# Optimization experiments

Hardware: AMD Instinct MI355X
Metric: run time of the kernel (lower is better)

Reference implementation:

```python
import jax, jax.numpy as jnp
import numpy as np
from math import sqrt

B, L, D, NH = 1, 2048, 1024, 16
HD = D // NH
EPS = 1e-5
NEG = -1e9


def setup_inputs() -> dict:
    key = jax.random.key(0)
    ks = jax.random.split(key, 5)
    x = jax.random.normal(ks[0], (B, L, D), jnp.float32)
    # causal additive mask (added to raw QK^T scores before /sqrt(d))
    causal = jnp.tril(jnp.ones((L, L), bool))
    m = jnp.where(causal, 0.0, NEG).astype(jnp.float32)[None, None]  # (1,1,L,L)
    init = lambda k, s: (0.02 * jax.random.normal(k, s)).astype(jnp.float32)
    return dict(
        x=x, m=m,
        wx_w=init(ks[1], (3 * D, D)), wx_b=jnp.zeros((3 * D,), jnp.float32),
        wo_w=init(ks[2], (D, D)), wo_b=jnp.zeros((D,), jnp.float32),
        ffn1_w=init(ks[3], (4 * D, D)), ffn1_b=jnp.zeros((4 * D,), jnp.float32),
        ffn2_w=init(ks[4], (D, 4 * D)), ffn2_b=jnp.zeros((D,), jnp.float32),
        ln1_w=jnp.float32(1.0), ln1_b=jnp.float32(0.0),
        ln2_w=jnp.float32(1.0), ln2_b=jnp.float32(0.0),
    )


def layer_norm(x, w, b):
    # scalar gain/bias, biased variance via E[x^2] - E[x]^2 (as in source)
    mu = x.mean(-1, keepdims=True)
    mu2 = (x * x).mean(-1, keepdims=True)
    sigma = jnp.sqrt(mu2 - mu * mu + EPS)
    return w * (x - mu) / sigma + b


def gelu(x):
    return x * 0.5 * (1 + jax.scipy.special.erf(x / sqrt(2.0)))


def reference(x, m, wx_w, wx_b, wo_w, wo_b, ffn1_w, ffn1_b, ffn2_w, ffn2_b,
              ln1_w, ln1_b, ln2_w, ln2_b):
    b, l, d = x.shape
    qkv = layer_norm(x, ln1_w, ln1_b) @ wx_w.T + wx_b          # (b,l,3d)
    q, k, v = [t.reshape(b, l, NH, HD) for t in jnp.split(qkv, 3, axis=-1)]
    # mask added BEFORE scaling by 1/sqrt(d) -- faithful to source
    scores = (jnp.einsum('bind,bjnd->bnij', q, k) + m) / sqrt(d)  # (b,nh,l,l)
    A = jax.nn.softmax(scores, axis=-1)
    mha = jnp.einsum('bnij,bjnd->bind', A, v).reshape(b, l, d)
    x = x + mha @ wo_w.T + wo_b
    h = layer_norm(x, ln2_w, ln2_b)
    return x + gelu(h @ ffn1_w.T + ffn1_b) @ ffn2_w.T + ffn2_b
```

## Files before the change

### kernel.cpp

```cpp
#include <hip/hip_runtime.h>

typedef short bf16x8 __attribute__((ext_vector_type(8)));
typedef float f32x4 __attribute__((ext_vector_type(4)));
typedef unsigned short u16;

__device__ __forceinline__ u16 f2b(float f) {
  unsigned u = __builtin_bit_cast(unsigned, f);
  u += 0x7fffu + ((u >> 16) & 1u);
  return (u16)(u >> 16);
}
__device__ __forceinline__ float b2f(u16 h) {
  unsigned u = ((unsigned)h) << 16;
  return __builtin_bit_cast(float, u);
}

__device__ __forceinline__ void gload16(const void* g, void* l) {
  __builtin_amdgcn_global_load_lds(
      (const __attribute__((address_space(1))) unsigned*)g,
      (__attribute__((address_space(3))) unsigned*)l, 16, 0, 0);
}

__global__ __launch_bounds__(256) void prep_kernel(
    const float* __restrict__ s0, int n0, const float* __restrict__ s1, int n1,
    const float* __restrict__ s2, int n2, const float* __restrict__ s3, int n3,
    u16* __restrict__ d0, u16* __restrict__ d1, u16* __restrict__ d2, u16* __restrict__ d3,
    const float* __restrict__ x, u16* __restrict__ lnout,
    const float* __restrict__ wp, const float* __restrict__ bp) {
  __shared__ float red[8];
  if (blockIdx.x < 1024) {
    long long total = ((long long)n0 + n1 + n2 + n3) >> 2;
    long long stride = 1024LL * 256;
    for (long long i = (long long)blockIdx.x * 256 + threadIdx.x; i < total; i += stride) {
      long long e = i << 2;
      const float* sp; u16* dp; long long off;
      if (e < n0)                { sp = s0; dp = d0; off = e; }
      else if (e < n0 + n1)      { sp = s1; dp = d1; off = e - n0; }
      else if (e < n0 + n1 + n2) { sp = s2; dp = d2; off = e - n0 - n1; }
      else                       { sp = s3; dp = d3; off = e - n0 - n1 - n2; }
      float4 v = *(const float4*)(sp + off);
      ushort4 o;
      o.x = f2b(v.x); o.y = f2b(v.y); o.z = f2b(v.z); o.w = f2b(v.w);
      *(ushort4*)(dp + off) = o;
    }
    return;
  }
  int row = blockIdx.x - 1024;
  const float* xr = x + (size_t)row * 1024;
  float4 v = ((const float4*)xr)[threadIdx.x];
  float lsum = v.x + v.y + v.z + v.w;
  float lsq = v.x * v.x + v.y * v.y + v.z * v.z + v.w * v.w;
#pragma unroll
  for (int off = 32; off; off >>= 1) {
    lsum += __shfl_down(lsum, off);
    lsq += __shfl_down(lsq, off);
  }
  int wv_ = threadIdx.x >> 6, ln_ = threadIdx.x & 63;
  if (ln_ == 0) { red[wv_] = lsum; red[4 + wv_] = lsq; }
  __syncthreads();
  if (threadIdx.x == 0) {
    float ts = red[0] + red[1] + red[2] + red[3];
    float ts2 = red[4] + red[5] + red[6] + red[7];
    red[0] = ts; red[4] = ts2;
  }
  __syncthreads();
  float mu = red[0] * (1.0f / 1024.0f);
  float mu2 = red[4] * (1.0f / 1024.0f);
  float inv = 1.0f / sqrtf(mu2 - mu * mu + 1e-5f);
  float gw = *wp, gb = *bp;
  ushort4 o;
  o.x = f2b(gw * (v.x - mu) * inv + gb);
  o.y = f2b(gw * (v.y - mu) * inv + gb);
  o.z = f2b(gw * (v.z - mu) * inv + gb);
  o.w = f2b(gw * (v.w - mu) * inv + gb);
  ((ushort4*)lnout)[(size_t)row * 256 + threadIdx.x] = o;
}

__global__ __launch_bounds__(256) void reduce2(
    const float* __restrict__ p, const float* __restrict__ bias,
    const float* __restrict__ resid, float* __restrict__ out) {
  int i = blockIdx.x * 256 + threadIdx.x;
  float4 a = ((const float4*)p)[i];
  float4 b = ((const float4*)p)[i + 524288];
  float4 r = ((const float4*)resid)[i];
  float4 bb = ((const float4*)bias)[i & 255];
  float4 o;
  o.x = a.x + b.x + r.x + bb.x;
  o.y = a.y + b.y + r.y + bb.y;
  o.z = a.z + b.z + r.z + bb.z;
  o.w = a.w + b.w + r.w + bb.w;
  ((float4*)out)[i] = o;
}

__global__ __launch_bounds__(256) void reduce_ln(
    const float* __restrict__ p, const float* __restrict__ bias,
    const float* __restrict__ resid, float* __restrict__ x1out,
    u16* __restrict__ lnout,
    const float* __restrict__ wp, const float* __restrict__ bp) {
  int row = blockIdx.x;
  int i = row * 256 + threadIdx.x;
  float4 a = ((const float4*)p)[i];
  float4 b = ((const float4*)p)[i + 524288];
  float4 r = ((const float4*)resid)[i];
  float4 bb = ((const float4*)bias)[threadIdx.x];
  float4 v;
  v.x = a.x + b.x + r.x + bb.x;
  v.y = a.y + b.y + r.y + bb.y;
  v.z = a.z + b.z + r.z + bb.z;
  v.w = a.w + b.w + r.w + bb.w;
  ((float4*)x1out)[i] = v;
  float lsum = v.x + v.y + v.z + v.w;
  float lsq = v.x * v.x + v.y * v.y + v.z * v.z + v.w * v.w;
#pragma unroll
  for (int off = 32; off; off >>= 1) {
    lsum += __shfl_down(lsum, off);
    lsq += __shfl_down(lsq, off);
  }
  __shared__ float red[8];
  int wv_ = threadIdx.x >> 6, ln_ = threadIdx.x & 63;
  if (ln_ == 0) { red[wv_] = lsum; red[4 + wv_] = lsq; }
  __syncthreads();
  if (threadIdx.x == 0) {
    float ts = red[0] + red[1] + red[2] + red[3];
    float ts2 = red[4] + red[5] + red[6] + red[7];
    red[0] = ts; red[4] = ts2;
  }
  __syncthreads();
  float mu = red[0] * (1.0f / 1024.0f);
  float mu2 = red[4] * (1.0f / 1024.0f);
  float inv = 1.0f / sqrtf(mu2 - mu * mu + 1e-5f);
  float gw = *wp, gb = *bp;
  ushort4 o;
  o.x = f2b(gw * (v.x - mu) * inv + gb);
  o.y = f2b(gw * (v.y - mu) * inv + gb);
  o.z = f2b(gw * (v.z - mu) * inv + gb);
  o.w = f2b(gw * (v.w - mu) * inv + gb);
  ((ushort4*)lnout)[i] = o;
}

#define BN 128
#define BK 64

template <int EPI, int BMT, bool SPLITX>
__global__ __launch_bounds__(256, (BMT == 128 ? 2 : 3)) void gemm_bt(
    const u16* __restrict__ A, const u16* __restrict__ W,
    const float* __restrict__ bias, const float* __restrict__ resid,
    void* __restrict__ Cout, u16* __restrict__ vtout, int M, int N, int K) {
  constexpr int MR = BMT / 32;
  __shared__ __align__(16) u16 sA[2][BMT * BK];
  __shared__ __align__(16) u16 sB[2][BN * BK];
  const int tid = threadIdx.x;

  const int gx = gridDim.x, gy = gridDim.y;
  int bx, by;
  {
    int oxy = blockIdx.y * gx + blockIdx.x;
    int xcd = oxy & 7, pos = oxy >> 3;
    if (SPLITX) {
      int bxp = gx >> 3;
      bx = xcd * bxp + pos % bxp;
      by = pos / bxp;
    } else {
      int byp = gy >> 3;
      by = xcd * byp + pos % byp;
      bx = pos / byp;
    }
  }

  const int l = tid & 63;
  const int w = tid >> 6;
  const int wm = w >> 1, wn = w & 1;
  const int lr = l & 15, lg = l >> 4;

  f32x4 acc[MR][4] = {};

  const int r_st = tid >> 3;
  const int s_st = tid & 7;

  const u16* Abase = A + (size_t)(by * BMT) * K;
  const u16* Wbase = W + (size_t)(bx * BN) * K;
  const int NK = K / (BK * (int)gridDim.z);
  const int ktbase = (int)blockIdx.z * NK;

  auto stage = [&](int buf, int kt) {
    const int k0 = (ktbase + kt) * BK;
#pragma unroll
    for (int i = 0; i < BMT / 32; i++) {
      int r = i * 32 + r_st;
      int ss = s_st ^ (r & 7);
      gload16(Abase + (size_t)r * K + k0 + ss * 8, &sA[buf][(i * 256 + tid) * 8]);
    }
#pragma unroll
    for (int i = 0; i < 4; i++) {
      int r = i * 32 + r_st;
      int ss = s_st ^ (r & 7);
      gload16(Wbase + (size_t)r * K + k0 + ss * 8, &sB[buf][(i * 256 + tid) * 8]);
    }
  };

  auto compute = [&](int buf) {
#pragma unroll
    for (int kk = 0; kk < 2; kk++) {
      bf16x8 a[MR], b[4];
#pragma unroll
      for (int mr = 0; mr < MR; mr++) {
        int row = wm * (BMT / 2) + mr * 16 + lr;
        int ss = (kk * 4 + lg) ^ (row & 7);
        a[mr] = *(const bf16x8*)&sA[buf][row * 64 + ss * 8];
      }
#pragma unroll
      for (int nr = 0; nr < 4; nr++) {
        int row = wn * 64 + nr * 16 + lr;
        int ss = (kk * 4 + lg) ^ (row & 7);
        b[nr] = *(const bf16x8*)&sB[buf][row * 64 + ss * 8];
      }
#pragma unroll
      for (int mr = 0; mr < MR; mr++)
#pragma unroll
        for (int nr = 0; nr < 4; nr++)
          acc[mr][nr] = __builtin_amdgcn_mfma_f32_16x16x32_bf16(a[mr], b[nr], acc[mr][nr], 0, 0, 0);
    }
  };

  stage(0, 0);
  asm volatile("s_waitcnt vmcnt(0)" ::: "memory");
  __syncthreads();
  for (int kt = 0; kt < NK; kt++) {
    if (kt + 1 < NK) stage((kt + 1) & 1, kt + 1);
    compute(kt & 1);
    asm volatile("s_waitcnt vmcnt(0)" ::: "memory");
    __syncthreads();
  }

  const int crow0 = by * BMT + wm * (BMT / 2);
  const int ccol0 = bx * BN + wn * 64;

  if (EPI == 4) {
    float* P4 = (float*)Cout + (size_t)blockIdx.z * (size_t)M * N;
#pragma unroll
    for (int nr = 0; nr < 4; nr++) {
      int col = ccol0 + nr * 16 + lr;
#pragma unroll
      for (int mr = 0; mr < MR; mr++) {
        int rowb = crow0 + mr * 16 + lg * 4;
#pragma unroll
        for (int r = 0; r < 4; r++)
          P4[(size_t)(rowb + r) * N + col] = acc[mr][nr][r];
      }
    }
    return;
  }

  if (EPI == 3 && ccol0 >= 2048) {
    const int hd0 = ccol0 - 2048;
#pragma unroll
    for (int nr = 0; nr < 4; nr++) {
      int hd = hd0 + nr * 16 + lr;
      float bv = bias[ccol0 + nr * 16 + lr];
#pragma unroll
      for (int mr = 0; mr < MR; mr++) {
        int m0 = crow0 + mr * 16 + lg * 4;
        ushort4 o;
        o.x = f2b(acc[mr][nr][0] + bv);
        o.y = f2b(acc[mr][nr][1] + bv);
        o.z = f2b(acc[mr][nr][2] + bv);
        o.w = f2b(acc[mr][nr][3] + bv);
        *(ushort4*)&vtout[(size_t)hd * 2048 + m0] = o;
      }
    }
    return;
  }

#pragma unroll
  for (int nr = 0; nr < 4; nr++) {
    int col = ccol0 + nr * 16 + lr;
    float bv = bias[col];
#pragma unroll
    for (int mr = 0; mr < MR; mr++) {
      int rowb = crow0 + mr * 16 + lg * 4;
#pragma unroll
      for (int r = 0; r < 4; r++) {
        float v = acc[mr][nr][r] + bv;
        size_t off = (size_t)(rowb + r) * N + col;
        if (EPI == 2) {
          float u = 0.7978845608f * (v + 0.044715f * v * v * v);
          u = fminf(15.0f, fmaxf(-15.0f, u));
          float e = __expf(2.0f * u);
          float g = 0.5f * v * (1.0f + (e - 1.0f) / (e + 1.0f));
          ((u16*)Cout)[off] = f2b(g);
        } else {
          ((u16*)Cout)[off] = f2b(v);
        }
      }
    }
  }
}

__global__ __launch_bounds__(256) void attn_kernel(
    const u16* __restrict__ qkv, const u16* __restrict__ vt,
    float* __restrict__ O0, float* __restrict__ O1, float* __restrict__ O2v,
    float* __restrict__ l0p, float* __restrict__ l1p, float* __restrict__ l2p) {
  const int i = (int)blockIdx.x;
  int qb, sec, nsec;
  if (i < 24)      { qb = 31 - i / 3;        sec = i % 3;        nsec = 3; }
  else if (i < 48) { qb = 23 - (i - 24) / 2; sec = (i - 24) & 1; nsec = 2; }
  else             { qb = 59 - i;            sec = 0;            nsec = 1; }
  const int nt = qb + 1;
  const int t0 = (nt * sec) / nsec;
  const int t1 = (nt * (sec + 1)) / nsec;

  const int h = blockIdx.y;
  __shared__ __align__(16) u16 sK[2][64 * 64];
  __shared__ __align__(16) u16 sV[2][64 * 64];
  __shared__ __align__(16) u16 P[4][16 * 72];
  const int tid = threadIdx.x;
  const int l = tid & 63, w = tid >> 6;
  const int lr = l & 15, lg = l >> 4;
  const int qrow0 = qb * 64 + w * 16;
  const u16* kbase = qkv + 1024 + h * 64;
  const u16* vbase = vt + (size_t)(h * 64) * 2048;

  const int r_st = tid >> 3;
  const int s_st = tid & 7;

  auto stage = [&](int buf, int t) {
    const int j0 = t * 64;
#pragma unroll
    for (int i2 = 0; i2 < 2; i2++) {
      int r = i2 * 32 + r_st;
      int ss = s_st ^ (r & 7);
      gload16(kbase + (size_t)(j0 + r) * 3072 + ss * 8, &sK[buf][(i2 * 256 + tid) * 8]);
    }
#pragma unroll
    for (int i2 = 0; i2 < 2; i2++) {
      int r = i2 * 32 + r_st;
      int ss = s_st ^ (r & 7);
      gload16(vbase + (size_t)r * 2048 + j0 + ss * 8, &sV[buf][(i2 * 256 + tid) * 8]);
    }
  };

  bf16x8 aq[2];
#pragma unroll
  for (int kk = 0; kk < 2; kk++)
    aq[kk] = *(const bf16x8*)&qkv[(size_t)(qrow0 + lr) * 3072 + h * 64 + kk * 32 + lg * 8];

  f32x4 oa[4];
  float l_r[4] = {0.f, 0.f, 0.f, 0.f};
#pragma unroll
  for (int d = 0; d < 4; d++) oa[d] = f32x4{0.f, 0.f, 0.f, 0.f};

  auto compute = [&](int buf, int t, bool masked) {
    const int j0 = t * 64;
    f32x4 s[4] = {};
#pragma unroll
    for (int kk = 0; kk < 2; kk++) {
#pragma unroll
      for (int c = 0; c < 4; c++) {
        int row = c * 16 + lr;
        int ss = (kk * 4 + lg) ^ (row & 7);
        bf16x8 kf = *(const bf16x8*)&sK[buf][row * 64 + ss * 8];
        s[c] = __builtin_amdgcn_mfma_f32_16x16x32_bf16(aq[kk], kf, s[c], 0, 0, 0);
      }
    }

#pragma unroll
    for (int r = 0; r < 4; r++) {
      const int q = qrow0 + lg * 4 + r;
      float rs = 0.f;
#pragma unroll
      for (int c = 0; c < 4; c++) {
        float p = __expf(s[c][r] * 0.03125f);
        if (masked) {
          int j = j0 + c * 16 + lr;
          p = (j > q) ? 0.f : p;
        }
        u16 pb = f2b(p);
        P[w][(lg * 4 + r) * 72 + c * 16 + lr] = pb;
        rs += b2f(pb);
      }
      l_r[r] += rs;
    }

#pragma unroll
    for (int kk = 0; kk < 2; kk++) {
      bf16x8 pa = *(const bf16x8*)&P[w][lr * 72 + kk * 32 + lg * 8];
#pragma unroll
      for (int d = 0; d < 4; d++) {
        int row = d * 16 + lr;
        int ss = (kk * 4 + lg) ^ (row & 7);
        bf16x8 bv = *(const bf16x8*)&sV[buf][row * 64 + ss * 8];
        oa[d] = __builtin_amdgcn_mfma_f32_16x16x32_bf16(pa, bv, oa[d], 0, 0, 0);
      }
    }
  };

  const int ntile = t1 - t0;
  stage(0, t0);
  asm volatile("s_waitcnt vmcnt(0)" ::: "memory");
  __syncthreads();
  for (int ti = 0; ti < ntile; ti++) {
    const int t = t0 + ti;
    if (ti + 1 < ntile) stage((ti + 1) & 1, t + 1);
    compute(ti & 1, t, t == nt - 1);
    asm volatile("s_waitcnt vmcnt(0)" ::: "memory");
    __syncthreads();
  }

  float* Op = (sec == 0) ? O0 : (sec == 1) ? O1 : O2v;
  float* lp = (sec == 0) ? l0p : (sec == 1) ? l1p : l2p;
#pragma unroll
  for (int r = 0; r < 4; r++) {
#pragma unroll
    for (int off = 1; off < 16; off <<= 1) l_r[r] += __shfl_xor(l_r[r], off);
    int q = qrow0 + lg * 4 + r;
    if (lr == 0) lp[q * 16 + h] = l_r[r];
#pragma unroll
    for (int d = 0; d < 4; d++)
      Op[(size_t)q * 1024 + h * 64 + d * 16 + lr] = oa[d][r];
  }
}

__global__ __launch_bounds__(256) void attn_combine(
    const float* __restrict__ O0, const float* __restrict__ O1,
    const float* __restrict__ O2v,
    const float* __restrict__ l0p, const float* __restrict__ l1p,
    const float* __restrict__ l2p, u16* __restrict__ mhab) {
  const int row = blockIdx.x;
  const int t = threadIdx.x;
  const int h = t >> 4;
  float4 v = ((const float4*)(O0 + (size_t)row * 1024))[t];
  float ls = l0p[row * 16 + h];
  if (row >= 768) {
    float4 v1 = ((const float4*)(O1 + (size_t)row * 1024))[t];
    v.x += v1.x; v.y += v1.y; v.z += v1.z; v.w += v1.w;
    ls += l1p[row * 16 + h];
  }
  if (row >= 1536) {
    float4 v2 = ((const float4*)(O2v + (size_t)row * 1024))[t];
    v.x += v2.x; v.y += v2.y; v.z += v2.z; v.w += v2.w;
    ls += l2p[row * 16 + h];
  }
  float inv = 1.0f / ls;
  ushort4 o;
  o.x = f2b(v.x * inv); o.y = f2b(v.y * inv);
  o.z = f2b(v.z * inv); o.w = f2b(v.w * inv);
  ((ushort4*)(mhab + (size_t)row * 1024))[t] = o;
}

extern "C" void kernel_launch(void* const* d_in, const int* in_sizes, int n_in,
                              void* d_out, int out_size, void* d_ws, size_t ws_size,
                              hipStream_t stream) {
  const float* x    = (const float*)d_in[0];
  const float* wx_w = (const float*)d_in[2];
  const float* wx_b = (const float*)d_in[3];
  const float* wo_w = (const float*)d_in[4];
  const float* wo_b = (const float*)d_in[5];
  const float* f1_w = (const float*)d_in[6];
  const float* f1_b = (const float*)d_in[7];
  const float* f2_w = (const float*)d_in[8];
  const float* f2_b = (const float*)d_in[9];
  const float* ln1w = (const float*)d_in[10];
  const float* ln1b = (const float*)d_in[11];
  const float* ln2w = (const float*)d_in[12];
  const float* ln2b = (const float*)d_in[13];

  char* ws = (char*)d_ws;
  u16*   ln_x  = (u16*)(ws + 0);
  float* l0p   = (float*)(ws + 0);
  float* l1p   = (float*)(ws + 131072);
  float* l2p   = (float*)(ws + 262144);
  u16*   qkv   = (u16*)(ws + 4194304);
  float* part  = (float*)(ws + 0);
  u16*   mhab  = (u16*)(ws + 16777216);
  float* x1    = (float*)(ws + 20971520);
  float* O0    = (float*)(ws + 20971520);
  u16*   hbuf  = (u16*)(ws + 29360128);
  u16*   vt    = (u16*)(ws + 33554432);
  u16*   f1o   = (u16*)(ws + 33554432);
  float* O1    = (float*)(ws + 37748736);
  float* O2v   = (float*)(ws + 46137344) - (size_t)1536 * 1024;
  u16*   wxb16 = (u16*)(ws + 50331648);
  u16*   wob16 = (u16*)(ws + 56623104);
  u16*   f1b16 = (u16*)(ws + 58720256);
  u16*   f2b16 = (u16*)(ws + 67108864);

  prep_kernel<<<3072, 256, 0, stream>>>(wx_w, 3145728, wo_w, 1048576, f1_w, 4194304, f2_w, 4194304,
                                        wxb16, wob16, f1b16, f2b16, x, ln_x, ln1w, ln1b);
  gemm_bt<3, 128, true><<<dim3(24, 16), 256, 0, stream>>>(ln_x, wxb16, wx_b, nullptr, qkv, vt, 2048, 3072, 1024);
  attn_kernel<<<dim3(60, 16), 256, 0, stream>>>(qkv, vt, O0, O1, O2v, l0p, l1p, l2p);
  attn_combine<<<2048, 256, 0, stream>>>(O0, O1, O2v, l0p, l1p, l2p, mhab);
  gemm_bt<4, 64, false><<<dim3(8, 32, 2), 256, 0, stream>>>(mhab, wob16, wo_b, nullptr, part, nullptr, 2048, 1024, 1024);
  reduce_ln<<<2048, 256, 0, stream>>>(part, wo_b, x, x1, hbuf, ln2w, ln2b);
  gemm_bt<2, 128, true><<<dim3(32, 16), 256, 0, stream>>>(hbuf, f1b16, f1_b, nullptr, f1o, nullptr, 2048, 4096, 1024);
  gemm_bt<4, 64, false><<<dim3(8, 32, 2), 256, 0, stream>>>(f1o, f2b16, f2_b, nullptr, part, nullptr, 2048, 1024, 4096);
  reduce2<<<2048, 256, 0, stream>>>(part, f2_b, x1, (float*)d_out);
}
```

Baseline: 153.7 us.

## Fuse fp32-to-bf16 weight conversion into QKV and FFN1 GEMM B-tile staging

The QKV and FFN1 GEMMs now read fp32 weights directly, convert them to bf16 in registers and write swizzled tiles to LDS, so the prep kernel no longer pre-converts those two weight matrices. This removes a separate conversion pass that read and wrote about 7M weight elements. In exchange, each GEMM block reads fp32 weights (twice the bytes), each weight tile is re-read and re-converted by every M-block, and B staging becomes a register round trip instead of direct global-to-LDS loads. That adds VGPR pressure and puts conversion work in the main loop.

Result: slower. 185.6 us (+20.8%).

```diff
diff --git a/kernel.cpp b/kernel.cpp
--- a/kernel.cpp
+++ b/kernel.cpp
@@ -22,21 +22,18 @@
 
 __global__ __launch_bounds__(256) void prep_kernel(
     const float* __restrict__ s0, int n0, const float* __restrict__ s1, int n1,
-    const float* __restrict__ s2, int n2, const float* __restrict__ s3, int n3,
-    u16* __restrict__ d0, u16* __restrict__ d1, u16* __restrict__ d2, u16* __restrict__ d3,
+    u16* __restrict__ d0, u16* __restrict__ d1,
     const float* __restrict__ x, u16* __restrict__ lnout,
     const float* __restrict__ wp, const float* __restrict__ bp) {
   __shared__ float red[8];
   if (blockIdx.x < 1024) {
-    long long total = ((long long)n0 + n1 + n2 + n3) >> 2;
+    long long total = ((long long)n0 + n1) >> 2;
     long long stride = 1024LL * 256;
     for (long long i = (long long)blockIdx.x * 256 + threadIdx.x; i < total; i += stride) {
       long long e = i << 2;
       const float* sp; u16* dp; long long off;
-      if (e < n0)                { sp = s0; dp = d0; off = e; }
-      else if (e < n0 + n1)      { sp = s1; dp = d1; off = e - n0; }
-      else if (e < n0 + n1 + n2) { sp = s2; dp = d2; off = e - n0 - n1; }
-      else                       { sp = s3; dp = d3; off = e - n0 - n1 - n2; }
+      if (e < n0) { sp = s0; dp = d0; off = e; }
+      else        { sp = s1; dp = d1; off = e - n0; }
       float4 v = *(const float4*)(sp + off);
       ushort4 o;
       o.x = f2b(v.x); o.y = f2b(v.y); o.z = f2b(v.z); o.w = f2b(v.w);
@@ -140,9 +137,10 @@
 #define BN 128
 #define BK 64
 
-template <int EPI, int BMT, bool SPLITX>
+template <int EPI, int BMT, bool SPLITX, bool BF32>
 __global__ __launch_bounds__(256, (BMT == 128 ? 2 : 3)) void gemm_bt(
-    const u16* __restrict__ A, const u16* __restrict__ W,
+    const u16* __restrict__ A, const u16* __restrict__ Wb,
+    const float* __restrict__ Wf,
     const float* __restrict__ bias, const float* __restrict__ resid,
     void* __restrict__ Cout, u16* __restrict__ vtout, int M, int N, int K) {
   constexpr int MR = BMT / 32;
@@ -177,11 +175,16 @@
   const int s_st = tid & 7;
 
   const u16* Abase = A + (size_t)(by * BMT) * K;
-  const u16* Wbase = W + (size_t)(bx * BN) * K;
+  const u16* Wbbase = BF32 ? nullptr : (Wb + (size_t)(bx * BN) * K);
+  const float* Wfbase = BF32 ? (Wf + (size_t)(bx * BN) * K) : nullptr;
   const int NK = K / (BK * (int)gridDim.z);
   const int ktbase = (int)blockIdx.z * NK;
 
-  auto stage = [&](int buf, int kt) {
+  const int browf = tid >> 1;
+  const int hh = tid & 1;
+  f32x4 breg[8];
+
+  auto stageA = [&](int buf, int kt) {
     const int k0 = (ktbase + kt) * BK;
 #pragma unroll
     for (int i = 0; i < BMT / 32; i++) {
@@ -189,11 +192,33 @@
       int ss = s_st ^ (r & 7);
       gload16(Abase + (size_t)r * K + k0 + ss * 8, &sA[buf][(i * 256 + tid) * 8]);
     }
+  };
+  auto stageB_g = [&](int buf, int kt) {
+    const int k0 = (ktbase + kt) * BK;
 #pragma unroll
     for (int i = 0; i < 4; i++) {
       int r = i * 32 + r_st;
       int ss = s_st ^ (r & 7);
-      gload16(Wbase + (size_t)r * K + k0 + ss * 8, &sB[buf][(i * 256 + tid) * 8]);
+      gload16(Wbbase + (size_t)r * K + k0 + ss * 8, &sB[buf][(i * 256 + tid) * 8]);
+    }
+  };
+  auto stageB_load = [&](int kt) {
+    const int k0 = (ktbase + kt) * BK;
+    const float* src = Wfbase + (size_t)browf * K + k0 + hh * 32;
+#pragma unroll
+    for (int j = 0; j < 8; j++) breg[j] = *(const f32x4*)(src + j * 4);
+  };
+  auto stageB_write = [&](int buf) {
+#pragma unroll
+    for (int j = 0; j < 4; j++) {
+      bf16x8 pk;
+#pragma unroll
+      for (int e = 0; e < 4; e++) {
+        pk[e] = (short)f2b(breg[2 * j][e]);
+        pk[4 + e] = (short)f2b(breg[2 * j + 1][e]);
+      }
+      int slot = (hh * 4 + j) ^ (browf & 7);
+      *(bf16x8*)&sB[buf][browf * 64 + slot * 8] = pk;
     }
   };
 
@@ -221,14 +246,30 @@
     }
   };
 
-  stage(0, 0);
-  asm volatile("s_waitcnt vmcnt(0)" ::: "memory");
-  __syncthreads();
-  for (int kt = 0; kt < NK; kt++) {
-    if (kt + 1 < NK) stage((kt + 1) & 1, kt + 1);
-    compute(kt & 1);
+  if (BF32) {
+    stageA(0, 0);
+    stageB_load(0);
+    asm volatile("s_waitcnt vmcnt(0)" ::: "memory");
+    stageB_write(0);
+    __syncthreads();
+    for (int kt = 0; kt < NK; kt++) {
+      if (kt + 1 < NK) { stageA((kt + 1) & 1, kt + 1); stageB_load(kt + 1); }
+      compute(kt & 1);
+      asm volatile("s_waitcnt vmcnt(0)" ::: "memory");
+      if (kt + 1 < NK) stageB_write((kt + 1) & 1);
+      __syncthreads();
+    }
+  } else {
+    stageA(0, 0);
+    stageB_g(0, 0);
     asm volatile("s_waitcnt vmcnt(0)" ::: "memory");
     __syncthreads();
+    for (int kt = 0; kt < NK; kt++) {
+      if (kt + 1 < NK) { stageA((kt + 1) & 1, kt + 1); stageB_g((kt + 1) & 1, kt + 1); }
+      compute(kt & 1);
+      asm volatile("s_waitcnt vmcnt(0)" ::: "memory");
+      __syncthreads();
+    }
   }
 
   const int crow0 = by * BMT + wm * (BMT / 2);
@@ -478,19 +519,21 @@
   u16*   f1o   = (u16*)(ws + 33554432);
   float* O1    = (float*)(ws + 37748736);
   float* O2v   = (float*)(ws + 46137344) - (size_t)1536 * 1024;
-  u16*   wxb16 = (u16*)(ws + 50331648);
   u16*   wob16 = (u16*)(ws + 56623104);
-  u16*   f1b16 = (u16*)(ws + 58720256);
   u16*   f2b16 = (u16*)(ws + 67108864);
 
-  prep_kernel<<<3072, 256, 0, stream>>>(wx_w, 3145728, wo_w, 1048576, f1_w, 4194304, f2_w, 4194304,
-                                        wxb16, wob16, f1b16, f2b16, x, ln_x, ln1w, ln1b);
-  gemm_bt<3, 128, true><<<dim3(24, 16), 256, 0, stream>>>(ln_x, wxb16, wx_b, nullptr, qkv, vt, 2048, 3072, 1024);
+  prep_kernel<<<3072, 256, 0, stream>>>(wo_w, 1048576, f2_w, 4194304,
+                                        wob16, f2b16, x, ln_x, ln1w, ln1b);
+  gemm_bt<3, 128, true, true><<<dim3(24, 16), 256, 0, stream>>>(
+      ln_x, nullptr, wx_w, wx_b, nullptr, qkv, vt, 2048, 3072, 1024);
   attn_kernel<<<dim3(60, 16), 256, 0, stream>>>(qkv, vt, O0, O1, O2v, l0p, l1p, l2p);
   attn_combine<<<2048, 256, 0, stream>>>(O0, O1, O2v, l0p, l1p, l2p, mhab);
-  gemm_bt<4, 64, false><<<dim3(8, 32, 2), 256, 0, stream>>>(mhab, wob16, wo_b, nullptr, part, nullptr, 2048, 1024, 1024);
+  gemm_bt<4, 64, false, false><<<dim3(8, 32, 2), 256, 0, stream>>>(
+      mhab, wob16, nullptr, wo_b, nullptr, part, nullptr, 2048, 1024, 1024);
   reduce_ln<<<2048, 256, 0, stream>>>(part, wo_b, x, x1, hbuf, ln2w, ln2b);
-  gemm_bt<2, 128, true><<<dim3(32, 16), 256, 0, stream>>>(hbuf, f1b16, f1_b, nullptr, f1o, nullptr, 2048, 4096, 1024);
-  gemm_bt<4, 64, false><<<dim3(8, 32, 2), 256, 0, stream>>>(f1o, f2b16, f2_b, nullptr, part, nullptr, 2048, 1024, 4096);
+  gemm_bt<2, 128, true, true><<<dim3(32, 16), 256, 0, stream>>>(
+      hbuf, nullptr, f1_w, f1_b, nullptr, f1o, nullptr, 2048, 4096, 1024);
+  gemm_bt<4, 64, false, false><<<dim3(8, 32, 2), 256, 0, stream>>>(
+      f1o, f2b16, nullptr, f2_b, nullptr, part, nullptr, 2048, 1024, 4096);
   reduce2<<<2048, 256, 0, stream>>>(part, f2_b, x1, (float*)d_out);
 }
```
